# Kernel tuning notes

Hardware: AMD Instinct MI355X
Metric: run time of the kernel (lower is better)

Reference implementation:

```python
import jax, jax.numpy as jnp
import numpy as np

BATCH, SEQ, D_IN = 4, 2048, 1024
STATE, D_OUT, KX = 1024, 1024, 10


def setup_inputs() -> dict:
    key = jax.random.key(0)
    k0, k1, k2, k3, k4, k5 = jax.random.split(key, 6)
    inputs = jax.random.normal(k0, (BATCH, SEQ, D_IN), jnp.float32)
    h0 = jax.random.normal(k1, (STATE,), jnp.float32)
    A = jax.random.normal(k2, (STATE,), jnp.float32)
    A = A / jnp.max(jnp.abs(A))  # matches init_A / max|init_A|
    B = jax.random.normal(k3, (D_IN, STATE), jnp.float32) / D_IN
    C = jax.random.normal(k4, (STATE, D_OUT), jnp.float32) / STATE
    M = jax.random.normal(k5, (D_IN, D_OUT, KX), jnp.float32) / D_OUT
    return {"inputs": inputs, "h0": h0, "A": A, "B": B, "C": C, "M": M}


def compute_ar_x_preds(w, x):
    # w: (d_out, d_in, k); x: (b, l, d_in)
    d_out, d_in, k = w.shape
    b, l, _ = x.shape
    o = jnp.einsum('oik,bli->bklo', w, x)  # (b, k, l, d_out)
    shifts = jnp.arange(k)
    # roll slice i forward by i along the length axis
    o = jax.vmap(lambda oi, s: jnp.roll(oi, s, axis=1), in_axes=(1, 0), out_axes=1)(o, shifts)
    # triu mask: keep position t in slice i only if t >= i (causal AR)
    m = (jnp.arange(l)[None, :] >= shifts[:, None]).astype(o.dtype)  # (k, l)
    return jnp.sum(o * m[None, :, :, None], axis=1)  # (b, l, d_out)


def reference(inputs, h0, A, B, C, M):
    bsz = inputs.shape[0]
    h_init = jnp.broadcast_to(h0, (bsz, h0.shape[0]))  # h0.expand(bsz, state_dim)
    u_seq = jnp.swapaxes(inputs, 0, 1)  # (l, b, d_in)

    def step(h, u):
        h_new = A * h + u @ B  # diagonal recurrence
        return h_new, h_new

    _, hs = jax.lax.scan(step, h_init, u_seq)  # (l, b, state)
    all_h_t = jnp.swapaxes(hs, 0, 1)  # (b, l, state)
    lds_out = all_h_t @ C  # (b, l, d_out)
    ar = compute_ar_x_preds(M, inputs)
    return lds_out + ar
```

## Files before the change

kernel.cpp:

```cpp
#include <hip/hip_runtime.h>
#include <stdint.h>

typedef unsigned short u16;
typedef __attribute__((ext_vector_type(4))) float f32x4;
typedef __attribute__((ext_vector_type(8))) short s16x8;

#define BATCH 4
#define SEQ   2048
#define DIM   1024
#define KX    10
#define PAD   16
#define SEQP  (SEQ+PAD)

__device__ __forceinline__ u16 f2b(float f) {
    union { float f; uint32_t u; } v; v.f = f;
    uint32_t u = v.u + 0x7fffu + ((v.u >> 16) & 1u);
    return (u16)(u >> 16);
}
__device__ __forceinline__ float b2f(u16 h) {
    union { uint32_t u; float f; } v; v.u = ((uint32_t)h) << 16;
    return v.f;
}

__device__ __forceinline__ long swz(int n, int k) {
    return (((long)((n >> 4) * 32 + (k >> 5))) << 9)
         + ((((k >> 3) & 3) * 16 + (n & 15)) << 3) + (k & 7);
}

__device__ __forceinline__ void llds16(const u16* g, u16* l) {
    __builtin_amdgcn_global_load_lds(
        (const __attribute__((address_space(1))) uint32_t*)g,
        (__attribute__((address_space(3))) uint32_t*)l, 16, 0, 0);
}

#define PREP_X_END  8256
#define PREP_C_END  10304
#define PREP_M_END  14400

__global__ __launch_bounds__(256) void k_prep(
    const float* __restrict__ x, const float* __restrict__ B,
    const float* __restrict__ C, const float* __restrict__ M,
    u16* __restrict__ Xpad, u16* __restrict__ Btr, u16* __restrict__ Wall)
{
    __shared__ float tile[32][33];
    const int bid = blockIdx.x, tid = threadIdx.x;

    if (bid < PREP_X_END) {
        int idx = bid * 256 + tid;
        long e = (long)idx * 4;
        int i = (int)(e & 1023);
        int row = (int)(e >> 10);
        int t = row % SEQP;
        int b = row / SEQP;
        ushort4 o;
        if (t < PAD) {
            o.x = 0; o.y = 0; o.z = 0; o.w = 0;
        } else {
            const float4 v = *(const float4*)(x + (((long)(b * SEQ + (t - PAD)) << 10) + i));
            o.x = f2b(v.x); o.y = f2b(v.y); o.z = f2b(v.z); o.w = f2b(v.w);
        }
        *(ushort4*)(Xpad + ((long)row << 10) + i) = o;
    } else if (bid < PREP_C_END) {
        const int tb = bid - PREP_X_END;
        const float* in = (tb < 1024) ? B : C;
        u16* out = (tb < 1024) ? Btr : Wall;
        int lb = tb & 1023;
        int bx = lb & 31, by = lb >> 5;
        int tx = tid & 31, ty = tid >> 5;
#pragma unroll
        for (int j = 0; j < 4; j++)
            tile[ty + j * 8][tx] = in[(long)(by * 32 + ty + j * 8) * 1024 + bx * 32 + tx];
        __syncthreads();
#pragma unroll
        for (int j = 0; j < 4; j++) {
            int n = bx * 32 + ty + j * 8;
            int k = by * 32 + tx;
            out[swz(n, k)] = f2b(tile[tx][ty + j * 8]);
        }
    } else {
        int idx = (bid - PREP_C_END) * 256 + tid;
        int o = idx >> 10, i = idx & 1023;
        const float* src = M + (long)idx * KX;
        long base = swz(o, i);
#pragma unroll
        for (int k = 0; k < KX; k++)
            Wall[(((long)(k + 1)) << 20) + base] = f2b(src[k]);
    }
}


__global__ void k_scan1(const u16* __restrict__ U, const float* __restrict__ A,
                        float* __restrict__ F) {
    int s = blockIdx.x * 256 + threadIdx.x;
    int bc = blockIdx.y;
    int b = bc >> 4, c = bc & 15;
    float a = A[s];
    const u16* u = U + (((long)(b * SEQ + c * 128)) << 10) + s;
    float f = 0.f;
#pragma unroll 8
    for (int j = 0; j < 128; j++) f = fmaf(a, f, b2f(u[(long)j << 10]));
    F[((long)bc << 10) + s] = f;
}

__global__ void k_scan2(const float* __restrict__ F, const float* __restrict__ A,
                        const float* __restrict__ h0, float* __restrict__ Carry) {
    int idx = blockIdx.x * 256 + threadIdx.x;
    int b = idx >> 10, s = idx & 1023;
    float a = A[s];
    float a128 = a;
#pragma unroll
    for (int q = 0; q < 7; q++) a128 *= a128;
    float carry = h0[s];
#pragma unroll
    for (int c = 0; c < 16; c++) {
        long off = ((long)(b * 16 + c) << 10) + s;
        Carry[off] = carry;
        carry = fmaf(a128, carry, F[off]);
    }
}

__global__ void k_scan3(const u16* __restrict__ U, const float* __restrict__ A,
                        const float* __restrict__ Carry, u16* __restrict__ Hsw) {
    int s = blockIdx.x * 256 + threadIdx.x;
    int bc = blockIdx.y;
    int b = bc >> 4, c = bc & 15;
    float a = A[s];
    int r0 = b * SEQ + c * 128;
    long base = ((long)r0 << 10) + s;
    float h = Carry[((long)bc << 10) + s];
    long sw = (((long)(s >> 5)) << 9) + ((((s >> 3) & 3) * 16) << 3) + (s & 7);
#pragma unroll 8
    for (int j = 0; j < 128; j++) {
        h = fmaf(a, h, b2f(U[base + ((long)j << 10)]));
        int r = r0 + j;
        Hsw[(((long)(r >> 4) * 32) << 9) + ((r & 15) << 3) + sw] = f2b(h);
    }
}

template<int NG, int USE_H, int BF16_OUT>
__global__ __launch_bounds__(256, 2) void k_gemm(
    void* __restrict__ outv, const u16* __restrict__ Xpad,
    const u16* __restrict__ Hsw, const u16* __restrict__ W)
{
    __shared__ u16 Asl[144 * 64];

    const int tid  = threadIdx.x;
    const int wave = tid >> 6, lane = tid & 63;
    const int wm = wave >> 1, wn = wave & 1;
    const int quad = lane >> 4, l15 = lane & 15;

    const int bid  = blockIdx.x;
    const int col0 = (bid & 7) * 128;
    const int row0 = (bid >> 3) * 128;
    const int bb = row0 >> 11;
    const long Xrow0 = (long)bb * SEQP + PAD + (row0 & (SEQ - 1));
    const long XslabBase = (Xrow0 - 16) << 10;

    const int n4b = (col0 >> 4) + wn * 4;
    const int r4b = (row0 >> 4) + wm * 4;

    f32x4 acc[4][4];
#pragma unroll
    for (int i = 0; i < 4; i++)
#pragma unroll
        for (int j = 0; j < 4; j++)
            acc[i][j] = (f32x4){0.f, 0.f, 0.f, 0.f};

    s16x8 wf[2][8];
    s16x8 hf[USE_H ? 8 : 1];

    for (int k0 = 0; k0 < 1024; k0 += 64) {
        const int kc = k0 >> 5;

#pragma unroll
        for (int q = 0; q < 5; q++) {
            int iu = q * 4 + wave;
            if (iu < 18) {
                int u = iu * 64 + lane;
                int row = u >> 3;
                int kcs = (u & 7) ^ (row & 7);
                llds16(Xpad + XslabBase + ((long)row << 10) + k0 + kcs * 8,
                       &Asl[iu * 512]);
            }
        }
        {
            const u16* Wg = W + (((long)(USE_H ? 1 : 0)) << 20);
#pragma unroll
            for (int ni = 0; ni < 4; ni++)
#pragma unroll
                for (int kk = 0; kk < 2; kk++)
                    wf[0][ni * 2 + kk] = *(const s16x8*)
                        (Wg + (((long)((n4b + ni) * 32 + kc + kk)) << 9) + (lane << 3));
        }
        if (USE_H) {
#pragma unroll
            for (int mi = 0; mi < 4; mi++)
#pragma unroll
                for (int kk = 0; kk < 2; kk++)
                    hf[mi * 2 + kk] = *(const s16x8*)
                        (Hsw + (((long)((r4b + mi) * 32 + kc + kk)) << 9) + (lane << 3));
        }
        __syncthreads();

#pragma unroll
        for (int g = 0; g < NG; g++) {
            if (g + 1 < NG) {
                const int wsel = USE_H ? ((g + 1 == NG - 1) ? 0 : g + 2) : g + 1;
                const u16* Wg = W + (((long)wsel) << 20);
#pragma unroll
                for (int ni = 0; ni < 4; ni++)
#pragma unroll
                    for (int kk = 0; kk < 2; kk++)
                        wf[(g + 1) & 1][ni * 2 + kk] = *(const s16x8*)
                            (Wg + (((long)((n4b + ni) * 32 + kc + kk)) << 9) + (lane << 3));
            }

            const bool isH = USE_H && (g == NG - 1);
            s16x8 af[4][2];
            if (isH) {
#pragma unroll
                for (int mi = 0; mi < 4; mi++) {
                    af[mi][0] = hf[mi * 2];
                    af[mi][1] = hf[mi * 2 + 1];
                }
            } else {
                const int rbase = 16 - g;
                const int r7 = (l15 + rbase) & 7;
#pragma unroll
                for (int mi = 0; mi < 4; mi++) {
                    int arow = rbase + wm * 64 + mi * 16 + l15;
#pragma unroll
                    for (int kk = 0; kk < 2; kk++)
                        af[mi][kk] = *(const s16x8*)
                            &Asl[arow * 64 + (((kk * 4 + quad) ^ r7) << 3)];
                }
            }
#pragma unroll
            for (int mi = 0; mi < 4; mi++)
#pragma unroll
                for (int ni = 0; ni < 4; ni++) {
                    acc[mi][ni] = __builtin_amdgcn_mfma_f32_16x16x32_bf16(
                        af[mi][0], wf[g & 1][ni * 2 + 0], acc[mi][ni], 0, 0, 0);
                    acc[mi][ni] = __builtin_amdgcn_mfma_f32_16x16x32_bf16(
                        af[mi][1], wf[g & 1][ni * 2 + 1], acc[mi][ni], 0, 0, 0);
                }
        }
        __syncthreads();
    }

#pragma unroll
    for (int mi = 0; mi < 4; mi++) {
        int r = row0 + wm * 64 + mi * 16 + quad * 4;
#pragma unroll
        for (int ni = 0; ni < 4; ni++) {
            int c = col0 + wn * 64 + ni * 16 + l15;
            f32x4 v = acc[mi][ni];
            if (BF16_OUT) {
                u16* ob = (u16*)outv;
#pragma unroll
                for (int reg = 0; reg < 4; reg++)
                    ob[((long)(r + reg) << 10) + c] = f2b(v[reg]);
            } else {
                float* of = (float*)outv;
#pragma unroll
                for (int reg = 0; reg < 4; reg++)
                    of[((long)(r + reg) << 10) + c] = v[reg];
            }
        }
    }
}


extern "C" void kernel_launch(void* const* d_in, const int* in_sizes, int n_in,
                              void* d_out, int out_size, void* d_ws, size_t ws_size,
                              hipStream_t stream) {
    const float* x  = (const float*)d_in[0];
    const float* h0 = (const float*)d_in[1];
    const float* A  = (const float*)d_in[2];
    const float* B  = (const float*)d_in[3];
    const float* C  = (const float*)d_in[4];
    const float* M  = (const float*)d_in[5];
    float* out = (float*)d_out;

    char* ws = (char*)d_ws;
    u16*   Xpad  = (u16*)  (ws);
    u16*   Wall  = (u16*)  (ws + 16908288);
    u16*   Btr   = (u16*)  (ws + 39976960);
    u16*   Ubf   = (u16*)  (ws + 42074112);
    u16*   Hsw   = (u16*)  (ws + 58851328);
    float* F     = (float*)(ws + 75628544);
    float* Carry = (float*)(ws + 75890688);

    k_prep<<<dim3(PREP_M_END), dim3(256), 0, stream>>>(x, B, C, M, Xpad, Btr, Wall);

    k_gemm<1, 0, 1><<<dim3(512), dim3(256), 0, stream>>>(Ubf, Xpad, Hsw, Btr);

    k_scan1<<<dim3(4, 64), dim3(256), 0, stream>>>(Ubf, A, F);
    k_scan2<<<dim3(16), dim3(256), 0, stream>>>(F, A, h0, Carry);
    k_scan3<<<dim3(4, 64), dim3(256), 0, stream>>>(Ubf, A, Carry, Hsw);

    k_gemm<11, 1, 0><<<dim3(512), dim3(256), 0, stream>>>(out, Xpad, Hsw, Wall);
}
```

Baseline: 338.2 us.

## Double-buffer X slab in LDS and prefetch next k-step operands across iterations

The GEMM main loop now uses two LDS buffers for the input slab. The next k-step's slab is issued asynchronously while the current one is consumed, and the next step's first weight fragment and H fragments are prefetched during the current step. This drops one barrier per iteration and hides global-to-LDS latency behind MFMA work. The cost is doubled LDS use (about 36 KB per block), which may limit occupancy under the 2-blocks-per-CU launch bound, plus extra register pressure from the prefetched fragments.

```diff
diff --git a/kernel.cpp b/kernel.cpp
--- a/kernel.cpp
+++ b/kernel.cpp
@@ -11,6 +11,8 @@
 #define KX    10
 #define PAD   16
 #define SEQP  (SEQ+PAD)
+
+template<int V> struct Int { static constexpr int value = V; };
 
 __device__ __forceinline__ u16 f2b(float f) {
     union { float f; uint32_t u; } v; v.f = f;
@@ -142,7 +144,7 @@
     void* __restrict__ outv, const u16* __restrict__ Xpad,
     const u16* __restrict__ Hsw, const u16* __restrict__ W)
 {
-    __shared__ u16 Asl[144 * 64];
+    __shared__ u16 Asl[2][144 * 64];
 
     const int tid  = threadIdx.x;
     const int wave = tid >> 6, lane = tid & 63;
@@ -169,9 +171,7 @@
     s16x8 wf[2][8];
     s16x8 hf[USE_H ? 8 : 1];
 
-    for (int k0 = 0; k0 < 1024; k0 += 64) {
-        const int kc = k0 >> 5;
-
+    auto stage_slab = [&](int k0, int buf) {
 #pragma unroll
         for (int q = 0; q < 5; q++) {
             int iu = q * 4 + wave;
@@ -180,40 +180,46 @@
                 int row = u >> 3;
                 int kcs = (u & 7) ^ (row & 7);
                 llds16(Xpad + XslabBase + ((long)row << 10) + k0 + kcs * 8,
-                       &Asl[iu * 512]);
+                       &Asl[buf][iu * 512]);
             }
         }
-        {
-            const u16* Wg = W + (((long)(USE_H ? 1 : 0)) << 20);
-#pragma unroll
-            for (int ni = 0; ni < 4; ni++)
-#pragma unroll
-                for (int kk = 0; kk < 2; kk++)
-                    wf[0][ni * 2 + kk] = *(const s16x8*)
-                        (Wg + (((long)((n4b + ni) * 32 + kc + kk)) << 9) + (lane << 3));
-        }
-        if (USE_H) {
-#pragma unroll
-            for (int mi = 0; mi < 4; mi++)
-#pragma unroll
-                for (int kk = 0; kk < 2; kk++)
-                    hf[mi * 2 + kk] = *(const s16x8*)
-                        (Hsw + (((long)((r4b + mi) * 32 + kc + kk)) << 9) + (lane << 3));
-        }
-        __syncthreads();
+    };
+    auto load_wf = [&](int k0, int g, s16x8* dst) {
+        const int wsel = USE_H ? ((g == NG - 1) ? 0 : g + 1) : g;
+        const u16* Wg = W + (((long)wsel) << 20);
+        const int kc = k0 >> 5;
+#pragma unroll
+        for (int ni = 0; ni < 4; ni++)
+#pragma unroll
+            for (int kk = 0; kk < 2; kk++)
+                dst[ni * 2 + kk] = *(const s16x8*)
+                    (Wg + (((long)((n4b + ni) * 32 + kc + kk)) << 9) + (lane << 3));
+    };
+    auto load_hf = [&](int k0) {
+        const int kc = k0 >> 5;
+#pragma unroll
+        for (int mi = 0; mi < 4; mi++)
+#pragma unroll
+            for (int kk = 0; kk < 2; kk++)
+                hf[mi * 2 + kk] = *(const s16x8*)
+                    (Hsw + (((long)((r4b + mi) * 32 + kc + kk)) << 9) + (lane << 3));
+    };
+
+    stage_slab(0, 0);
+    load_wf(0, 0, wf[0]);
+    if (USE_H) load_hf(0);
+    __syncthreads();
+
+    auto body = [&](int k0, auto pc) {
+        constexpr int P = decltype(pc)::value;
+        const bool more = (k0 + 64) < 1024;
+        if (more) stage_slab(k0 + 64, P ^ 1);
 
 #pragma unroll
         for (int g = 0; g < NG; g++) {
-            if (g + 1 < NG) {
-                const int wsel = USE_H ? ((g + 1 == NG - 1) ? 0 : g + 2) : g + 1;
-                const u16* Wg = W + (((long)wsel) << 20);
-#pragma unroll
-                for (int ni = 0; ni < 4; ni++)
-#pragma unroll
-                    for (int kk = 0; kk < 2; kk++)
-                        wf[(g + 1) & 1][ni * 2 + kk] = *(const s16x8*)
-                            (Wg + (((long)((n4b + ni) * 32 + kc + kk)) << 9) + (lane << 3));
-            }
+            const int p = (P + g) & 1;
+            if (g + 1 < NG)      load_wf(k0, g + 1, wf[p ^ 1]);
+            else if (more)       load_wf(k0 + 64, 0, wf[p ^ 1]);
 
             const bool isH = USE_H && (g == NG - 1);
             s16x8 af[4][2];
@@ -223,6 +229,7 @@
                     af[mi][0] = hf[mi * 2];
                     af[mi][1] = hf[mi * 2 + 1];
                 }
+                if (more) load_hf(k0 + 64);
             } else {
                 const int rbase = 16 - g;
                 const int r7 = (l15 + rbase) & 7;
@@ -232,7 +239,7 @@
 #pragma unroll
                     for (int kk = 0; kk < 2; kk++)
                         af[mi][kk] = *(const s16x8*)
-                            &Asl[arow * 64 + (((kk * 4 + quad) ^ r7) << 3)];
+                            &Asl[P][arow * 64 + (((kk * 4 + quad) ^ r7) << 3)];
                 }
             }
 #pragma unroll
@@ -240,12 +247,17 @@
 #pragma unroll
                 for (int ni = 0; ni < 4; ni++) {
                     acc[mi][ni] = __builtin_amdgcn_mfma_f32_16x16x32_bf16(
-                        af[mi][0], wf[g & 1][ni * 2 + 0], acc[mi][ni], 0, 0, 0);
+                        af[mi][0], wf[p][ni * 2 + 0], acc[mi][ni], 0, 0, 0);
                     acc[mi][ni] = __builtin_amdgcn_mfma_f32_16x16x32_bf16(
-                        af[mi][1], wf[g & 1][ni * 2 + 1], acc[mi][ni], 0, 0, 0);
+                        af[mi][1], wf[p][ni * 2 + 1], acc[mi][ni], 0, 0, 0);
                 }
         }
         __syncthreads();
+    };
+
+    for (int k0 = 0; k0 < 1024; k0 += 128) {
+        body(k0,      Int<0>{});
+        body(k0 + 64, Int<1>{});
     }
 
 #pragma unroll
```

Measured after the change: 338.1 us. About the same (-0.0%).
